# Optimization experiments

Hardware: AMD Instinct MI355X
Metric: run time of the kernel (lower is better)

## Reference

```python
import jax, jax.numpy as jnp
import numpy as np

N = 262144      # total tokens
LM1 = 6         # max digit chars after the first character
D = 128         # embedding_dim
NUM_LAB = 1000
V1 = 2 * 26 + NUM_LAB  # first-level table rows (1052)


def setup_inputs() -> dict:
    key = jax.random.key(0)
    k1, k2, k3, k4, k5, k6, k7 = jax.random.split(key, 7)
    return {
        "first_chars": jax.random.randint(k1, (N,), 0, 26, dtype=jnp.int32),
        "digits": jax.random.randint(k2, (N, LM1), 0, 10, dtype=jnp.int32),
        "ndigits": jax.random.randint(k3, (N,), 0, 7, dtype=jnp.int32),
        "mods": jax.random.randint(k4, (N,), 0, 3, dtype=jnp.int32),  # 0=icd10,1=atc,2=lab
        "vals": jax.random.normal(k5, (N,), dtype=jnp.float32),
        "E1": jax.random.normal(k6, (V1, D), dtype=jnp.float32),
        "Eint": jax.random.normal(k7, (10, D), dtype=jnp.float32),
        "kappa": 2,
    }


def reference(first_chars, digits, ndigits, mods, vals, E1, Eint, kappa):
    # first-level index per modality: icd -> c+5, atc -> 2c+5, lab -> 52+code
    first_idx = jnp.where(
        mods == 0, first_chars + 5,
        jnp.where(mods == 1, first_chars * 2 + 5, 52 + first_chars))
    base = E1[first_idx]                                  # [N, D]

    # position-decayed digit accumulation: sum_i 1/(i+2)^kappa * Eint[digit_i]
    pos = jnp.arange(LM1, dtype=jnp.float32)
    w = 1.0 / (pos + 2.0) ** kappa                        # [LM1]
    mask = (jnp.arange(LM1)[None, :] < ndigits[:, None]).astype(base.dtype)
    onehot = jax.nn.one_hot(digits, 10, dtype=base.dtype)  # [N, LM1, 10]
    digit_emb = jnp.einsum("nl,nlk,kd->nd", w[None, :] * mask, onehot, Eint)

    # modality scatter: lab tokens use base * val, icd/atc use base + decayed digits
    final = jnp.where((mods == 2)[:, None], base * vals[:, None], base + digit_emb)
    return final
```

## Files before the change

kernel.cpp:

```cpp
#include <hip/hip_runtime.h>
#include <hip/hip_bf16.h>


#define LM1 6
#define D   128
#define TPB 128
#define TPT 4
#define NCHUNK (TPB / 32)

typedef float nfloat4 __attribute__((ext_vector_type(4)));

__global__ __launch_bounds__(256) void hier_emb_kernel(
    const int*   __restrict__ first_chars,
    const int*   __restrict__ digits,
    const int*   __restrict__ ndigits,
    const int*   __restrict__ mods,
    const float* __restrict__ vals,
    const float* __restrict__ E1,
    const float* __restrict__ Eint,
    const int*   __restrict__ kappa_p,
    float*       __restrict__ out,
    int n)
{
    __shared__ float sEint[10][D];
    __shared__ int   sFidx[TPB];
    __shared__ int   sNd[TPB];
    __shared__ int   sMod[TPB];
    __shared__ float sVal[TPB];
    __shared__ int   sDig[TPB * LM1];

    const int tid  = threadIdx.x;
    const int tok0 = blockIdx.x * TPB;

    {
        const nfloat4* src = reinterpret_cast<const nfloat4*>(Eint);
        nfloat4*       dst = reinterpret_cast<nfloat4*>(&sEint[0][0]);
        dst[tid] = src[tid];
        const int i2 = 256 + tid;
        if (i2 < (10 * D) / 4) dst[i2] = src[i2];
    }

    if (tid < TPB) {
        int tt = tok0 + tid; if (tt >= n) tt = n - 1;
        const int mod = mods[tt];
        const int fc  = first_chars[tt];
        sMod[tid]  = mod;
        sFidx[tid] = (mod == 0) ? (fc + 5) : (mod == 1) ? (fc * 2 + 5) : (52 + fc);
        sNd[tid]   = ndigits[tt];
        sVal[tid]  = vals[tt];
    }
    {
        const long lim = (long)n * LM1;
#pragma unroll
        for (int r = 0; r < (TPB * LM1) / 256; ++r) {
            const int i = tid + r * 256;
            long gi = (long)tok0 * LM1 + i;
            if (gi >= lim) gi = lim - 1;
            sDig[i] = digits[gi];
        }
    }

    const int k = *kappa_p;
    float w[LM1];
#pragma unroll
    for (int i = 0; i < LM1; ++i) {
        float p = 1.0f;
        const float b = (float)(i + 2);
        for (int j = 0; j < k; ++j) p *= b;
        w[i] = 1.0f / p;
    }

    __syncthreads();

    const int q  = tid & 31;
    const int g  = tid >> 5;

#pragma unroll 2
    for (int c = 0; c < NCHUNK; ++c) {
        const int ltb = c * 32 + g * TPT;

        nfloat4 base[TPT];
#pragma unroll
        for (int j = 0; j < TPT; ++j) {
            const int fidx = sFidx[ltb + j];
            base[j] = *reinterpret_cast<const nfloat4*>(E1 + (size_t)fidx * D + q * 4);
        }

        nfloat4 acc[TPT];
#pragma unroll
        for (int j = 0; j < TPT; ++j) {
            const int lt  = ltb + j;
            const int mod = sMod[lt];
            if (mod == 2) {
                acc[j] = base[j] * sVal[lt];
            } else {
                acc[j] = base[j];
                const int nd = sNd[lt];
#pragma unroll
                for (int i = 0; i < LM1; ++i) {
                    if (i < nd) {
                        const int dg = sDig[lt * LM1 + i];
                        const nfloat4 e =
                            *reinterpret_cast<const nfloat4*>(&sEint[dg][q * 4]);
                        acc[j] += w[i] * e;
                    }
                }
            }
        }

#pragma unroll
        for (int j = 0; j < TPT; ++j) {
            const int tok = tok0 + ltb + j;
            if (tok < n) {
                __builtin_nontemporal_store(
                    acc[j],
                    reinterpret_cast<nfloat4*>(out + (size_t)tok * D + q * 4));
            }
        }
    }
}

extern "C" void kernel_launch(void* const* d_in, const int* in_sizes, int n_in,
                              void* d_out, int out_size, void* d_ws, size_t ws_size,
                              hipStream_t stream) {
    const int*   first_chars = (const int*)  d_in[0];
    const int*   digits      = (const int*)  d_in[1];
    const int*   ndigits     = (const int*)  d_in[2];
    const int*   mods        = (const int*)  d_in[3];
    const float* vals        = (const float*)d_in[4];
    const float* E1          = (const float*)d_in[5];
    const float* Eint        = (const float*)d_in[6];
    const int*   kappa       = (const int*)  d_in[7];
    float*       out         = (float*)d_out;

    const int n    = in_sizes[0];
    const int grid = (n + TPB - 1) / TPB;

    hier_emb_kernel<<<grid, 256, 0, stream>>>(
        first_chars, digits, ndigits, mods, vals, E1, Eint, kappa, out, n);
}
```

Before: 165.4 us.

## Cache E1 icd/atc rows in LDS and interleave token-to-wave mapping

Stages the 52 E1 rows used by icd/atc tokens (indices 5..56) into shared memory, so only lab tokens fetch base rows from global memory. The token assignment changes so each 64-lane wave covers two tokens per step (half-waves interleaved), which alters divergence between the mod==2 and non-lab paths. Adds a launch-bounds occupancy hint. In exchange, every block pays extra LDS (about 26KB) and a 52-row preload, which may reduce occupancy on a memory-bound kernel dominated by output writes.

```diff
diff --git a/kernel.cpp b/kernel.cpp
--- a/kernel.cpp
+++ b/kernel.cpp
@@ -7,10 +7,12 @@
 #define TPB 128
 #define TPT 4
 #define NCHUNK (TPB / 32)
+#define E1LO   5
+#define E1ROWS 52
 
 typedef float nfloat4 __attribute__((ext_vector_type(4)));
 
-__global__ __launch_bounds__(256) void hier_emb_kernel(
+__global__ __launch_bounds__(256, 4) void hier_emb_kernel(
     const int*   __restrict__ first_chars,
     const int*   __restrict__ digits,
     const int*   __restrict__ ndigits,
@@ -22,6 +24,7 @@
     float*       __restrict__ out,
     int n)
 {
+    __shared__ float sE1[E1ROWS][D];
     __shared__ float sEint[10][D];
     __shared__ int   sFidx[TPB];
     __shared__ int   sNd[TPB];
@@ -33,13 +36,21 @@
     const int tok0 = blockIdx.x * TPB;
 
     {
+        const nfloat4* src = reinterpret_cast<const nfloat4*>(E1 + E1LO * D);
+        nfloat4*       dst = reinterpret_cast<nfloat4*>(&sE1[0][0]);
+#pragma unroll
+        for (int r = 0; r < 7; ++r) {
+            const int i = tid + r * 256;
+            if (i < (E1ROWS * D) / 4) dst[i] = src[i];
+        }
+    }
+    {
         const nfloat4* src = reinterpret_cast<const nfloat4*>(Eint);
         nfloat4*       dst = reinterpret_cast<nfloat4*>(&sEint[0][0]);
         dst[tid] = src[tid];
         const int i2 = 256 + tid;
         if (i2 < (10 * D) / 4) dst[i2] = src[i2];
     }
-
     if (tid < TPB) {
         int tt = tok0 + tid; if (tt >= n) tt = n - 1;
         const int mod = mods[tt];
@@ -73,48 +84,52 @@
     __syncthreads();
 
     const int q  = tid & 31;
-    const int g  = tid >> 5;
+    const int h  = (tid >> 5) & 1;
+    const int wv = tid >> 6;
 
 #pragma unroll 2
     for (int c = 0; c < NCHUNK; ++c) {
-        const int ltb = c * 32 + g * TPT;
+        int     lt[TPT];
+        nfloat4 base[TPT];
 
-        nfloat4 base[TPT];
 #pragma unroll
         for (int j = 0; j < TPT; ++j) {
-            const int fidx = sFidx[ltb + j];
-            base[j] = *reinterpret_cast<const nfloat4*>(E1 + (size_t)fidx * D + q * 4);
+            lt[j] = c * 32 + wv * 8 + j * 2 + h;
+            if (sMod[lt[j]] == 2) {
+                const int fidx = sFidx[lt[j]];
+                base[j] = *reinterpret_cast<const nfloat4*>(
+                    E1 + (size_t)fidx * D + q * 4);
+            }
         }
-
-        nfloat4 acc[TPT];
 #pragma unroll
         for (int j = 0; j < TPT; ++j) {
-            const int lt  = ltb + j;
-            const int mod = sMod[lt];
-            if (mod == 2) {
-                acc[j] = base[j] * sVal[lt];
+            if (sMod[lt[j]] != 2) {
+                base[j] = *reinterpret_cast<const nfloat4*>(
+                    &sE1[sFidx[lt[j]] - E1LO][q * 4]);
+            }
+        }
+#pragma unroll
+        for (int j = 0; j < TPT; ++j) {
+            const int lt_ = lt[j];
+            nfloat4 acc;
+            if (sMod[lt_] == 2) {
+                acc = base[j] * sVal[lt_];
             } else {
-                acc[j] = base[j];
-                const int nd = sNd[lt];
+                acc = base[j];
+                const int nd = sNd[lt_];
 #pragma unroll
                 for (int i = 0; i < LM1; ++i) {
                     if (i < nd) {
-                        const int dg = sDig[lt * LM1 + i];
-                        const nfloat4 e =
-                            *reinterpret_cast<const nfloat4*>(&sEint[dg][q * 4]);
-                        acc[j] += w[i] * e;
+                        const int dg = sDig[lt_ * LM1 + i];
+                        acc += w[i] * *reinterpret_cast<const nfloat4*>(
+                                          &sEint[dg][q * 4]);
                     }
                 }
             }
-        }
-
-#pragma unroll
-        for (int j = 0; j < TPT; ++j) {
-            const int tok = tok0 + ltb + j;
+            const int tok = tok0 + lt_;
             if (tok < n) {
                 __builtin_nontemporal_store(
-                    acc[j],
-                    reinterpret_cast<nfloat4*>(out + (size_t)tok * D + q * 4));
+                    acc, reinterpret_cast<nfloat4*>(out + (size_t)tok * D + q * 4));
             }
         }
     }
```

Result: slower. 180.8 us (+9.3%).

## Pack token metadata into int4 and software-pipeline E1 row loads across tokens

Applied to the files above, without the earlier changes.

Token metadata (first-level index, packed 4-bit digits, digit count, value) is packed into one int4 shared entry. Lab tokens are folded into the same path: they get zero digits and their value, while other tokens get a scale of 1. This removes the per-token branch. The main loop is restructured so each thread handles two tokens per step and prefetches the next E1 rows while computing the current ones. Occupancy is hinted with launch bounds (256, 8). The cost is an extra barrier and a digit-packing pass.

```diff
diff --git a/kernel.cpp b/kernel.cpp
--- a/kernel.cpp
+++ b/kernel.cpp
@@ -5,12 +5,11 @@
 #define LM1 6
 #define D   128
 #define TPB 128
-#define TPT 4
-#define NCHUNK (TPB / 32)
 
 typedef float nfloat4 __attribute__((ext_vector_type(4)));
+typedef int   nint4   __attribute__((ext_vector_type(4)));
 
-__global__ __launch_bounds__(256) void hier_emb_kernel(
+__global__ __launch_bounds__(256, 8) void hier_emb_kernel(
     const int*   __restrict__ first_chars,
     const int*   __restrict__ digits,
     const int*   __restrict__ ndigits,
@@ -23,10 +22,7 @@
     int n)
 {
     __shared__ float sEint[10][D];
-    __shared__ int   sFidx[TPB];
-    __shared__ int   sNd[TPB];
-    __shared__ int   sMod[TPB];
-    __shared__ float sVal[TPB];
+    __shared__ nint4 sMeta[TPB];
     __shared__ int   sDig[TPB * LM1];
 
     const int tid  = threadIdx.x;
@@ -39,16 +35,6 @@
         const int i2 = 256 + tid;
         if (i2 < (10 * D) / 4) dst[i2] = src[i2];
     }
-
-    if (tid < TPB) {
-        int tt = tok0 + tid; if (tt >= n) tt = n - 1;
-        const int mod = mods[tt];
-        const int fc  = first_chars[tt];
-        sMod[tid]  = mod;
-        sFidx[tid] = (mod == 0) ? (fc + 5) : (mod == 1) ? (fc * 2 + 5) : (52 + fc);
-        sNd[tid]   = ndigits[tt];
-        sVal[tid]  = vals[tt];
-    }
     {
         const long lim = (long)n * LM1;
 #pragma unroll
@@ -58,6 +44,16 @@
             if (gi >= lim) gi = lim - 1;
             sDig[i] = digits[gi];
         }
+    }
+    if (tid < TPB) {
+        int tt = tok0 + tid; if (tt >= n) tt = n - 1;
+        const int mod  = mods[tt];
+        const int fc   = first_chars[tt];
+        const int fidx = (mod == 0) ? fc + 5 : (mod == 1) ? fc * 2 + 5 : 52 + fc;
+        const int nd   = (mod == 2) ? 0 : ndigits[tt];
+        const float v  = (mod == 2) ? vals[tt] : 1.0f;
+        nint4 m; m.x = fidx; m.y = 0; m.z = nd; m.w = __float_as_int(v);
+        sMeta[tid] = m;
     }
 
     const int k = *kappa_p;
@@ -72,51 +68,72 @@
 
     __syncthreads();
 
-    const int q  = tid & 31;
-    const int g  = tid >> 5;
+    if (tid < TPB) {
+        int pd = 0;
+#pragma unroll
+        for (int i = 0; i < LM1; ++i) pd |= sDig[tid * LM1 + i] << (4 * i);
+        reinterpret_cast<int*>(sMeta)[tid * 4 + 1] = pd;
+    }
+    __syncthreads();
 
-#pragma unroll 2
-    for (int c = 0; c < NCHUNK; ++c) {
-        const int ltb = c * 32 + g * TPT;
+    const int q4 = (tid & 31) * 4;
+    const int h  = (tid >> 5) & 1;
+    const int wv = tid >> 6;
+    const int tb = wv * 32;
 
-        nfloat4 base[TPT];
+    const float* E1Q   = E1 + q4;
+    const float* EintQ = &sEint[0][q4];
+    float*       outQ  = out + q4;
+
+
+    nint4 m0 = sMeta[tb + h];
+    nint4 m1 = sMeta[tb + h + 2];
+    nfloat4 b0 = *reinterpret_cast<const nfloat4*>(E1Q + (size_t)m0.x * D);
+    nfloat4 b1 = *reinterpret_cast<const nfloat4*>(E1Q + (size_t)m1.x * D);
+
 #pragma unroll
-        for (int j = 0; j < TPT; ++j) {
-            const int fidx = sFidx[ltb + j];
-            base[j] = *reinterpret_cast<const nfloat4*>(E1 + (size_t)fidx * D + q * 4);
+    for (int g = 0; g < 8; ++g) {
+        nint4 p0, p1; nfloat4 c0, c1;
+        if (g < 7) {
+            const int ln = tb + (g + 1) * 4 + h;
+            p0 = sMeta[ln];
+            p1 = sMeta[ln + 2];
+            c0 = *reinterpret_cast<const nfloat4*>(E1Q + (size_t)p0.x * D);
+            c1 = *reinterpret_cast<const nfloat4*>(E1Q + (size_t)p1.x * D);
         }
 
-        nfloat4 acc[TPT];
+        const int ltA = tb + g * 4 + h;
+        {
+            nfloat4 acc = b0 * __int_as_float(m0.w);
+            const int nd = m0.z, pd = m0.y;
 #pragma unroll
-        for (int j = 0; j < TPT; ++j) {
-            const int lt  = ltb + j;
-            const int mod = sMod[lt];
-            if (mod == 2) {
-                acc[j] = base[j] * sVal[lt];
-            } else {
-                acc[j] = base[j];
-                const int nd = sNd[lt];
-#pragma unroll
-                for (int i = 0; i < LM1; ++i) {
-                    if (i < nd) {
-                        const int dg = sDig[lt * LM1 + i];
-                        const nfloat4 e =
-                            *reinterpret_cast<const nfloat4*>(&sEint[dg][q * 4]);
-                        acc[j] += w[i] * e;
-                    }
+            for (int i = 0; i < LM1; ++i) {
+                if (i < nd) {
+                    const int dg = (pd >> (4 * i)) & 15;
+                    acc += w[i] * *reinterpret_cast<const nfloat4*>(EintQ + dg * D);
                 }
             }
+            const int tok = tok0 + ltA;
+            if (tok < n)
+                __builtin_nontemporal_store(
+                    acc, reinterpret_cast<nfloat4*>(outQ + (size_t)tok * D));
         }
-
+        {
+            nfloat4 acc = b1 * __int_as_float(m1.w);
+            const int nd = m1.z, pd = m1.y;
 #pragma unroll
-        for (int j = 0; j < TPT; ++j) {
-            const int tok = tok0 + ltb + j;
-            if (tok < n) {
+            for (int i = 0; i < LM1; ++i) {
+                if (i < nd) {
+                    const int dg = (pd >> (4 * i)) & 15;
+                    acc += w[i] * *reinterpret_cast<const nfloat4*>(EintQ + dg * D);
+                }
+            }
+            const int tok = tok0 + ltA + 2;
+            if (tok < n)
                 __builtin_nontemporal_store(
-                    acc[j],
-                    reinterpret_cast<nfloat4*>(out + (size_t)tok * D + q * 4));
-            }
+                    acc, reinterpret_cast<nfloat4*>(outQ + (size_t)tok * D));
         }
+        m0 = p0; m1 = p1; b0 = c0; b1 = c1;
     }
 }
 
```

Result: faster. 161.5 us (-2.4%).
